# Kernel optimization log

Measured on AMD Instinct MI355X. Metric: run time of the kernel, lower is better.

## Reference

```python
import jax, jax.numpy as jnp
import numpy as np
import math

HIDDEN = 512
NUM_HEADS = 16
HEAD_DIM = HIDDEN // NUM_HEADS          # 32
SPOW_DIM = HEAD_DIM * (HEAD_DIM + 1) // 2  # 528
GAMMA = 0.9
B, S = 2, 1024

_TRIU_I, _TRIU_J = np.triu_indices(HEAD_DIM, k=1)
_SQRT2 = math.sqrt(2.0)


def spow2(x):
    # x: (..., d) -> (..., d*(d+1)//2); squares then sqrt(2)*upper-tri cross terms
    squares = x * x
    cross = _SQRT2 * (x[..., _TRIU_I] * x[..., _TRIU_J])
    return jnp.concatenate([squares, cross], axis=-1)


def setup_inputs() -> dict:
    key = jax.random.key(0)
    ks = jax.random.split(key, 9)
    lim = 1.0 / math.sqrt(HIDDEN)
    w = lambda k: jax.random.uniform(k, (HIDDEN, HIDDEN), jnp.float32, -lim, lim)
    b = lambda k: jax.random.uniform(k, (HIDDEN,), jnp.float32, -lim, lim)
    return {
        "x": jax.random.normal(ks[0], (B, S, HIDDEN), jnp.float32),
        "q_w": w(ks[1]), "q_b": b(ks[2]),
        "k_w": w(ks[3]), "k_b": b(ks[4]),
        "v_w": w(ks[5]), "v_b": b(ks[6]),
        "o_w": w(ks[7]), "o_b": b(ks[8]),
    }


def reference(x, q_w, q_b, k_w, k_b, v_w, v_b, o_w, o_b):
    Bb, Ss, Hh = x.shape
    q = (x @ q_w + q_b).reshape(Bb, Ss, NUM_HEADS, HEAD_DIM)
    k = (x @ k_w + k_b).reshape(Bb, Ss, NUM_HEADS, HEAD_DIM)
    v = (x @ v_w + v_b).reshape(Bb, Ss, NUM_HEADS, HEAD_DIM)

    sq = spow2(q)  # [B,S,H,Dspow]
    sk = spow2(k)  # [B,S,H,Dspow]

    # time-major for scan
    sq_t = jnp.moveaxis(sq, 1, 0)  # [S,B,H,D]
    sk_t = jnp.moveaxis(sk, 1, 0)
    v_t = jnp.moveaxis(v, 1, 0)    # [S,B,H,hd]

    state0 = jnp.zeros((Bb, NUM_HEADS, SPOW_DIM, HEAD_DIM), x.dtype)

    def step(state, inp):
        skt, sqt, vt = inp
        # state = gamma*state + spow_k \otimes v  -> [B,H,Dspow,hd]
        state = GAMMA * state + skt[..., :, None] * vt[..., None, :]
        out = jnp.einsum('bhD,bhDd->bhd', sqt, state)
        return state, out

    _, outs = jax.lax.scan(step, state0, (sk_t, sq_t, v_t))  # [S,B,H,hd]
    out = jnp.moveaxis(outs, 0, 1).reshape(Bb, Ss, Hh)
    return out @ o_w + o_b
```

## Files before the change

### kernel.cpp

```cpp
#include <hip/hip_runtime.h>
#include <hip/hip_bf16.h>
#include <math.h>

#define HIDDEN 512
#define NHEADS 16
#define HDIM   32
#define BATCH  2
#define SEQ    1024
#define MROWS  (BATCH * SEQ)

constexpr float LOG2_GAMMA = -0.15200309344504997f;

typedef __hip_bfloat16 bf16;
typedef __attribute__((ext_vector_type(8))) short short8;
typedef __attribute__((ext_vector_type(4))) float f32x4;

__device__ __forceinline__ void async16(const void* g, void* l) {
    __builtin_amdgcn_global_load_lds(
        (const __attribute__((address_space(1))) void*)g,
        (__attribute__((address_space(3))) void*)l, 16, 0, 0);
}

__device__ __forceinline__ unsigned short f2bf_bits(float f) {
    bf16 b = __float2bfloat16(f);
    return *(unsigned short*)&b;
}

__global__ __launch_bounds__(256) void prep(
    const float* __restrict__ x,
    const float* __restrict__ qw, const float* __restrict__ kw,
    const float* __restrict__ vw, const float* __restrict__ ow,
    bf16* __restrict__ xb, bf16* __restrict__ wqkvt, bf16* __restrict__ wot)
{
    const int blk = blockIdx.x, tid = threadIdx.x;
    if (blk < 256) {
        const int widx = blk >> 6;
        const int tile = blk & 63;
        const int tk = (tile & 7) * 64, tn = (tile >> 3) * 64;
        const float* w = widx == 0 ? qw : widx == 1 ? kw : widx == 2 ? vw : ow;
        __shared__ float t[64][65];
        #pragma unroll
        for (int u = 0; u < 4; ++u) {
            const int r = u * 16 + (tid >> 4);
            const int c = (tid & 15) * 4;
            float4 v = *(const float4*)&w[(size_t)(tk + r) * 512 + tn + c];
            t[r][c + 0] = v.x; t[r][c + 1] = v.y; t[r][c + 2] = v.z; t[r][c + 3] = v.w;
        }
        __syncthreads();
        #pragma unroll
        for (int u = 0; u < 2; ++u) {
            const int rr = u * 32 + (tid >> 3);
            const int cc = (tid & 7) * 8;
            alignas(16) unsigned short tmp[8];
            #pragma unroll
            for (int i = 0; i < 8; ++i) tmp[i] = f2bf_bits(t[cc + i][rr]);
            bf16* dst = (widx < 3)
                ? &wqkvt[((size_t)widx * 512 + tn + rr) * 512 + tk + cc]
                : &wot[(size_t)(tn + rr) * 512 + tk + cc];
            *(short8*)dst = *(short8*)tmp;
        }
    } else {
        #pragma unroll
        for (int u = 0; u < 4; ++u) {
            const int idx = (blk - 256) * 1024 + u * 256 + tid;
            float4 v = ((const float4*)x)[idx];
            unsigned pk0 = (unsigned)f2bf_bits(v.x) | ((unsigned)f2bf_bits(v.y) << 16);
            unsigned pk1 = (unsigned)f2bf_bits(v.z) | ((unsigned)f2bf_bits(v.w) << 16);
            uint2 pk = {pk0, pk1};
            *(uint2*)&xb[(size_t)idx * 4] = pk;
        }
    }
}

template<int BM, int BN, int EPI>
__global__ __launch_bounds__(256) void gemm_mfma(
    const bf16* __restrict__ A, const bf16* __restrict__ Bt,
    const float* __restrict__ b0, const float* __restrict__ b1,
    const float* __restrict__ b2,
    float* __restrict__ Cf, bf16* __restrict__ Cb, int ldc)
{
    constexpr int K = 512, BK = 32;
    constexpr int TM = BM / 32, TN = BN / 32;
    __shared__ alignas(16) short As[BM * BK];
    __shared__ alignas(16) short Bs[BN * BK];

    const int tid = threadIdx.x;
    const int wave = tid >> 6, lane = tid & 63;
    const int m0 = blockIdx.y * BM, n0 = blockIdx.x * BN;
    const int wm = (wave >> 1) * (BM / 2), wn = (wave & 1) * (BN / 2);
    const int fr = lane & 15, quad = lane >> 4;
    const int fk = quad * 8;
    const int lrow = lane >> 2, lk = (lane & 3) * 8;

    f32x4 acc[TM][TN] = {};

    for (int k0 = 0; k0 < K; k0 += BK) {
        #pragma unroll
        for (int u = 0; u < BM / 64; ++u) {
            const int rb = (wave * (BM / 64) + u) * 16;
            async16(&A[(size_t)(m0 + rb + lrow) * K + k0 + lk], &As[rb * BK]);
        }
        #pragma unroll
        for (int u = 0; u < BN / 64; ++u) {
            const int rb = (wave * (BN / 64) + u) * 16;
            async16(&Bt[(size_t)(n0 + rb + lrow) * K + k0 + lk], &Bs[rb * BK]);
        }
        __syncthreads();

        short8 af[TM], bfr[TN];
        #pragma unroll
        for (int i = 0; i < TM; ++i)
            af[i] = *(const short8*)&As[(wm + i * 16 + fr) * BK + fk];
        #pragma unroll
        for (int j = 0; j < TN; ++j)
            bfr[j] = *(const short8*)&Bs[(wn + j * 16 + fr) * BK + fk];
        #pragma unroll
        for (int i = 0; i < TM; ++i)
            #pragma unroll
            for (int j = 0; j < TN; ++j)
                acc[i][j] = __builtin_amdgcn_mfma_f32_16x16x32_bf16(
                    af[i], bfr[j], acc[i][j], 0, 0, 0);
        __syncthreads();
    }

    if (EPI == 1) {
        const int seg = (blockIdx.x * BN) >> 9;
        const float* bp = seg == 0 ? b0 : seg == 1 ? b1 : b2;
        const float sgn = seg == 0 ? 0.5f : seg == 1 ? -0.5f : 0.0f;
        #pragma unroll
        for (int i = 0; i < TM; ++i) {
            const int mrow = m0 + wm + i * 16 + quad * 4;
            float sc[4];
            #pragma unroll
            for (int r = 0; r < 4; ++r)
                sc[r] = exp2f((float)((mrow + r) & 63) * (sgn * LOG2_GAMMA));
            #pragma unroll
            for (int j = 0; j < TN; ++j) {
                const int n = n0 + wn + j * 16 + fr;
                const float bv = bp[n & 511];
                #pragma unroll
                for (int r = 0; r < 4; ++r) {
                    unsigned short h = f2bf_bits((acc[i][j][r] + bv) * sc[r]);
                    *(unsigned short*)&Cb[(size_t)(mrow + r) * ldc + n] = h;
                }
            }
        }
    } else {
        #pragma unroll
        for (int i = 0; i < TM; ++i) {
            const int mrow = m0 + wm + i * 16 + quad * 4;
            #pragma unroll
            for (int j = 0; j < TN; ++j) {
                const int n = n0 + wn + j * 16 + fr;
                const float bv = b0[n];
                #pragma unroll
                for (int r = 0; r < 4; ++r)
                    Cf[(size_t)(mrow + r) * ldc + n] = acc[i][j][r] + bv;
            }
        }
    }
}

__global__ __launch_bounds__(256) void power_attn_mfma(
    const bf16* __restrict__ qkv, bf16* __restrict__ atc)
{
    __shared__ alignas(16) short Qs[64 * 32];
    __shared__ alignas(16) short Ks[64 * 32];
    __shared__ alignas(16) short Vt[32 * 80];
    __shared__ alignas(16) short Ps[64 * 72];

    const int tid = threadIdx.x, wave = tid >> 6, lane = tid & 63;
    const int chunk = blockIdx.x, bh = blockIdx.y;
    const int b = bh >> 4, h = bh & 15;
    const int mb = b * SEQ + chunk * 64;
    const int fr = lane & 15, quad = lane >> 4;

    async16(&qkv[(size_t)(mb + wave * 16 + (lane >> 2)) * 1536 + h * 32 + (lane & 3) * 8],
            &Qs[wave * 512]);

    f32x4 o0 = {}, o1 = {};
    const int jstart = chunk >= 2 ? chunk - 2 : 0;

    for (int j = jstart; j <= chunk; ++j) {
        __syncthreads();
        const int sb = b * SEQ + j * 64;
        async16(&qkv[(size_t)(sb + wave * 16 + (lane >> 2)) * 1536 + 512 + h * 32 + (lane & 3) * 8],
                &Ks[wave * 512]);
        if (tid < 128) {
            const int p = tid >> 2, s = p * 2, dbase = (tid & 3) * 8;
            const short* g = (const short*)&qkv[(size_t)(sb + s) * 1536 + 1024 + h * 32 + dbase];
            short8 v0 = *(const short8*)g;
            short8 v1 = *(const short8*)(g + 1536);
            #pragma unroll
            for (int i = 0; i < 8; ++i) {
                unsigned pk = (unsigned)(unsigned short)v0[i]
                            | ((unsigned)(unsigned short)v1[i] << 16);
                *(unsigned*)&Vt[(dbase + i) * 80 + s] = pk;
            }
        }
        __syncthreads();

        short8 aq = *(const short8*)&Qs[(wave * 16 + fr) * 32 + quad * 8];
        f32x4 sAcc[4] = {};
        #pragma unroll
        for (int nt = 0; nt < 4; ++nt) {
            short8 bk = *(const short8*)&Ks[(nt * 16 + fr) * 32 + quad * 8];
            sAcc[nt] = __builtin_amdgcn_mfma_f32_16x16x32_bf16(aq, bk, sAcc[nt], 0, 0, 0);
        }

        const int dj = chunk - j;
        const float sj = exp2f(64.0f * (float)dj * LOG2_GAMMA);
        const int tbase = wave * 16 + quad * 4;
        #pragma unroll
        for (int nt = 0; nt < 4; ++nt) {
            const int s_l = nt * 16 + fr;
            #pragma unroll
            for (int r = 0; r < 4; ++r) {
                const int t_l = tbase + r;
                float pv = sAcc[nt][r];
                pv = pv * pv * sj;
                if (dj == 0 && s_l > t_l) pv = 0.0f;
                Ps[t_l * 72 + s_l] = (short)f2bf_bits(pv);
            }
        }
        short8 a0 = *(const short8*)&Ps[(wave * 16 + fr) * 72 + quad * 8];
        short8 a1 = *(const short8*)&Ps[(wave * 16 + fr) * 72 + 32 + quad * 8];
        short8 b00 = *(const short8*)&Vt[fr * 80 + quad * 8];
        short8 b01 = *(const short8*)&Vt[fr * 80 + 32 + quad * 8];
        short8 b10 = *(const short8*)&Vt[(16 + fr) * 80 + quad * 8];
        short8 b11 = *(const short8*)&Vt[(16 + fr) * 80 + 32 + quad * 8];
        o0 = __builtin_amdgcn_mfma_f32_16x16x32_bf16(a0, b00, o0, 0, 0, 0);
        o0 = __builtin_amdgcn_mfma_f32_16x16x32_bf16(a1, b01, o0, 0, 0, 0);
        o1 = __builtin_amdgcn_mfma_f32_16x16x32_bf16(a0, b10, o1, 0, 0, 0);
        o1 = __builtin_amdgcn_mfma_f32_16x16x32_bf16(a1, b11, o1, 0, 0, 0);
    }

    #pragma unroll
    for (int r = 0; r < 4; ++r) {
        const size_t row = mb + wave * 16 + quad * 4 + r;
        const int col = h * 32 + fr;
        *(unsigned short*)&atc[row * 512 + col]      = f2bf_bits(o0[r]);
        *(unsigned short*)&atc[row * 512 + col + 16] = f2bf_bits(o1[r]);
    }
}

extern "C" void kernel_launch(void* const* d_in, const int* in_sizes, int n_in,
                              void* d_out, int out_size, void* d_ws, size_t ws_size,
                              hipStream_t stream)
{
    const float* x  = (const float*)d_in[0];
    const float* qw = (const float*)d_in[1];
    const float* qb = (const float*)d_in[2];
    const float* kw = (const float*)d_in[3];
    const float* kb = (const float*)d_in[4];
    const float* vw = (const float*)d_in[5];
    const float* vb = (const float*)d_in[6];
    const float* ow = (const float*)d_in[7];
    const float* ob = (const float*)d_in[8];
    float* out = (float*)d_out;

    char* w = (char*)d_ws;
    bf16* xb    = (bf16*)(w);
    bf16* wqkvt = (bf16*)(w + (2ull  << 20));
    bf16* wot   = (bf16*)(w + (2ull  << 20) + (1536ull << 10));
    bf16* qkvb  = (bf16*)(w + (4ull  << 20));
    bf16* atc   = (bf16*)(w + (10ull << 20));

    prep<<<512, 256, 0, stream>>>(x, qw, kw, vw, ow, xb, wqkvt, wot);

    gemm_mfma<128, 64, 1><<<dim3(1536 / 64, MROWS / 128), 256, 0, stream>>>(
        xb, wqkvt, qb, kb, vb, nullptr, qkvb, 1536);

    power_attn_mfma<<<dim3(SEQ / 64, BATCH * NHEADS), 256, 0, stream>>>(qkvb, atc);

    gemm_mfma<64, 64, 0><<<dim3(512 / 64, MROWS / 64), 256, 0, stream>>>(
        atc, wot, ob, nullptr, nullptr, out, nullptr, 512);
}
```

Measured before the change: 99.17 us.

## Load MFMA fragments directly from global memory instead of staging through LDS

Both GEMMs drop the LDS-staged tile loop with its barriers and instead have each wave load its bf16 A/B fragments straight from global memory into registers. The loop is fully unrolled and software-prefetches the next k-step. The QKV GEMM also moves to 64x64 tiles, which doubles its block count. The attention kernel now reads Q and K fragments directly from global instead of going through shared buffers. This removes LDS traffic and __syncthreads, but gives up intra-block data reuse, so more global and L2 reads are issued.

```diff
diff --git a/kernel.cpp b/kernel.cpp
--- a/kernel.cpp
+++ b/kernel.cpp
@@ -14,12 +14,6 @@
 typedef __hip_bfloat16 bf16;
 typedef __attribute__((ext_vector_type(8))) short short8;
 typedef __attribute__((ext_vector_type(4))) float f32x4;
-
-__device__ __forceinline__ void async16(const void* g, void* l) {
-    __builtin_amdgcn_global_load_lds(
-        (const __attribute__((address_space(1))) void*)g,
-        (__attribute__((address_space(3))) void*)l, 16, 0, 0);
-}
 
 __device__ __forceinline__ unsigned short f2bf_bits(float f) {
     bf16 b = __float2bfloat16(f);
@@ -72,71 +66,63 @@
     }
 }
 
-template<int BM, int BN, int EPI>
-__global__ __launch_bounds__(256) void gemm_mfma(
+template<int EPI>
+__global__ __launch_bounds__(256) void gemm_direct(
     const bf16* __restrict__ A, const bf16* __restrict__ Bt,
     const float* __restrict__ b0, const float* __restrict__ b1,
     const float* __restrict__ b2,
     float* __restrict__ Cf, bf16* __restrict__ Cb, int ldc)
 {
-    constexpr int K = 512, BK = 32;
-    constexpr int TM = BM / 32, TN = BN / 32;
-    __shared__ alignas(16) short As[BM * BK];
-    __shared__ alignas(16) short Bs[BN * BK];
-
+    constexpr int K = 512;
     const int tid = threadIdx.x;
     const int wave = tid >> 6, lane = tid & 63;
-    const int m0 = blockIdx.y * BM, n0 = blockIdx.x * BN;
-    const int wm = (wave >> 1) * (BM / 2), wn = (wave & 1) * (BN / 2);
     const int fr = lane & 15, quad = lane >> 4;
-    const int fk = quad * 8;
-    const int lrow = lane >> 2, lk = (lane & 3) * 8;
-
-    f32x4 acc[TM][TN] = {};
-
-    for (int k0 = 0; k0 < K; k0 += BK) {
-        #pragma unroll
-        for (int u = 0; u < BM / 64; ++u) {
-            const int rb = (wave * (BM / 64) + u) * 16;
-            async16(&A[(size_t)(m0 + rb + lrow) * K + k0 + lk], &As[rb * BK]);
-        }
-        #pragma unroll
-        for (int u = 0; u < BN / 64; ++u) {
-            const int rb = (wave * (BN / 64) + u) * 16;
-            async16(&Bt[(size_t)(n0 + rb + lrow) * K + k0 + lk], &Bs[rb * BK]);
-        }
-        __syncthreads();
-
-        short8 af[TM], bfr[TN];
-        #pragma unroll
-        for (int i = 0; i < TM; ++i)
-            af[i] = *(const short8*)&As[(wm + i * 16 + fr) * BK + fk];
-        #pragma unroll
-        for (int j = 0; j < TN; ++j)
-            bfr[j] = *(const short8*)&Bs[(wn + j * 16 + fr) * BK + fk];
-        #pragma unroll
-        for (int i = 0; i < TM; ++i)
-            #pragma unroll
-            for (int j = 0; j < TN; ++j)
-                acc[i][j] = __builtin_amdgcn_mfma_f32_16x16x32_bf16(
-                    af[i], bfr[j], acc[i][j], 0, 0, 0);
-        __syncthreads();
-    }
+    const int m0 = blockIdx.y * 64 + (wave >> 1) * 32;
+    const int n0 = blockIdx.x * 64 + (wave & 1) * 32;
+
+    const bf16* pa0 = &A[(size_t)(m0 + fr) * K + quad * 8];
+    const bf16* pa1 = pa0 + (size_t)16 * K;
+    const bf16* pb0 = &Bt[(size_t)(n0 + fr) * K + quad * 8];
+    const bf16* pb1 = pb0 + (size_t)16 * K;
+
+    f32x4 acc00 = {}, acc01 = {}, acc10 = {}, acc11 = {};
+    short8 ca0 = *(const short8*)pa0;
+    short8 ca1 = *(const short8*)pa1;
+    short8 cb0 = *(const short8*)pb0;
+    short8 cb1 = *(const short8*)pb1;
+
+    #pragma unroll
+    for (int ks = 0; ks < 16; ++ks) {
+        short8 na0, na1, nb0, nb1;
+        if (ks < 15) {
+            na0 = *(const short8*)(pa0 + (ks + 1) * 32);
+            na1 = *(const short8*)(pa1 + (ks + 1) * 32);
+            nb0 = *(const short8*)(pb0 + (ks + 1) * 32);
+            nb1 = *(const short8*)(pb1 + (ks + 1) * 32);
+        }
+        acc00 = __builtin_amdgcn_mfma_f32_16x16x32_bf16(ca0, cb0, acc00, 0, 0, 0);
+        acc01 = __builtin_amdgcn_mfma_f32_16x16x32_bf16(ca0, cb1, acc01, 0, 0, 0);
+        acc10 = __builtin_amdgcn_mfma_f32_16x16x32_bf16(ca1, cb0, acc10, 0, 0, 0);
+        acc11 = __builtin_amdgcn_mfma_f32_16x16x32_bf16(ca1, cb1, acc11, 0, 0, 0);
+        ca0 = na0; ca1 = na1; cb0 = nb0; cb1 = nb1;
+    }
+
+    f32x4 acc[2][2] = {{acc00, acc01}, {acc10, acc11}};
 
     if (EPI == 1) {
-        const int seg = (blockIdx.x * BN) >> 9;
+        const int seg = (blockIdx.x * 64) >> 9;
         const float* bp = seg == 0 ? b0 : seg == 1 ? b1 : b2;
         const float sgn = seg == 0 ? 0.5f : seg == 1 ? -0.5f : 0.0f;
         #pragma unroll
-        for (int i = 0; i < TM; ++i) {
-            const int mrow = m0 + wm + i * 16 + quad * 4;
+        for (int i = 0; i < 2; ++i) {
+            const int mrow = m0 + i * 16 + quad * 4;
             float sc[4];
             #pragma unroll
             for (int r = 0; r < 4; ++r)
                 sc[r] = exp2f((float)((mrow + r) & 63) * (sgn * LOG2_GAMMA));
             #pragma unroll
-            for (int j = 0; j < TN; ++j) {
-                const int n = n0 + wn + j * 16 + fr;
+            for (int j = 0; j < 2; ++j) {
+                const int n = n0 + j * 16 + fr;
                 const float bv = bp[n & 511];
                 #pragma unroll
                 for (int r = 0; r < 4; ++r) {
@@ -147,11 +133,11 @@
         }
     } else {
         #pragma unroll
-        for (int i = 0; i < TM; ++i) {
-            const int mrow = m0 + wm + i * 16 + quad * 4;
-            #pragma unroll
-            for (int j = 0; j < TN; ++j) {
-                const int n = n0 + wn + j * 16 + fr;
+        for (int i = 0; i < 2; ++i) {
+            const int mrow = m0 + i * 16 + quad * 4;
+            #pragma unroll
+            for (int j = 0; j < 2; ++j) {
+                const int n = n0 + j * 16 + fr;
                 const float bv = b0[n];
                 #pragma unroll
                 for (int r = 0; r < 4; ++r)
@@ -164,8 +150,6 @@
 __global__ __launch_bounds__(256) void power_attn_mfma(
     const bf16* __restrict__ qkv, bf16* __restrict__ atc)
 {
-    __shared__ alignas(16) short Qs[64 * 32];
-    __shared__ alignas(16) short Ks[64 * 32];
     __shared__ alignas(16) short Vt[32 * 80];
     __shared__ alignas(16) short Ps[64 * 72];
 
@@ -175,8 +159,7 @@
     const int mb = b * SEQ + chunk * 64;
     const int fr = lane & 15, quad = lane >> 4;
 
-    async16(&qkv[(size_t)(mb + wave * 16 + (lane >> 2)) * 1536 + h * 32 + (lane & 3) * 8],
-            &Qs[wave * 512]);
+    short8 aq = *(const short8*)&qkv[(size_t)(mb + wave * 16 + fr) * 1536 + h * 32 + quad * 8];
 
     f32x4 o0 = {}, o1 = {};
     const int jstart = chunk >= 2 ? chunk - 2 : 0;
@@ -184,8 +167,6 @@
     for (int j = jstart; j <= chunk; ++j) {
         __syncthreads();
         const int sb = b * SEQ + j * 64;
-        async16(&qkv[(size_t)(sb + wave * 16 + (lane >> 2)) * 1536 + 512 + h * 32 + (lane & 3) * 8],
-                &Ks[wave * 512]);
         if (tid < 128) {
             const int p = tid >> 2, s = p * 2, dbase = (tid & 3) * 8;
             const short* g = (const short*)&qkv[(size_t)(sb + s) * 1536 + 1024 + h * 32 + dbase];
@@ -200,11 +181,10 @@
         }
         __syncthreads();
 
-        short8 aq = *(const short8*)&Qs[(wave * 16 + fr) * 32 + quad * 8];
         f32x4 sAcc[4] = {};
         #pragma unroll
         for (int nt = 0; nt < 4; ++nt) {
-            short8 bk = *(const short8*)&Ks[(nt * 16 + fr) * 32 + quad * 8];
+            short8 bk = *(const short8*)&qkv[(size_t)(sb + nt * 16 + fr) * 1536 + 512 + h * 32 + quad * 8];
             sAcc[nt] = __builtin_amdgcn_mfma_f32_16x16x32_bf16(aq, bk, sAcc[nt], 0, 0, 0);
         }
 
@@ -268,11 +248,11 @@
 
     prep<<<512, 256, 0, stream>>>(x, qw, kw, vw, ow, xb, wqkvt, wot);
 
-    gemm_mfma<128, 64, 1><<<dim3(1536 / 64, MROWS / 128), 256, 0, stream>>>(
+    gemm_direct<1><<<dim3(1536 / 64, MROWS / 64), 256, 0, stream>>>(
         xb, wqkvt, qb, kb, vb, nullptr, qkvb, 1536);
 
     power_attn_mfma<<<dim3(SEQ / 64, BATCH * NHEADS), 256, 0, stream>>>(qkvb, atc);
 
-    gemm_mfma<64, 64, 0><<<dim3(512 / 64, MROWS / 64), 256, 0, stream>>>(
+    gemm_direct<0><<<dim3(512 / 64, MROWS / 64), 256, 0, stream>>>(
         atc, wot, ob, nullptr, nullptr, out, nullptr, 512);
 }
```

Measured after the change: 115.2 us. +16.1%, slower.

## Stage full-K B tile in LDS and stream A fragments directly from global

Applied to the files above, without the earlier changes.

Replaces the K-looped GEMM, which staged both A and B per 32-wide K step with two barriers each, by a kernel that loads the whole 64xK B slab into padded LDS once. A fragments are then read straight from global memory into registers with no further barriers. The goal is to remove per-step synchronization and LDS traffic for A. The cost is more LDS per block (about 66KB), which lowers occupancy, and uncoalesced 16-byte global A loads with no latency hiding from prefetch.

```diff
diff --git a/kernel.cpp b/kernel.cpp
--- a/kernel.cpp
+++ b/kernel.cpp
@@ -72,71 +72,64 @@
     }
 }
 
-template<int BM, int BN, int EPI>
-__global__ __launch_bounds__(256) void gemm_mfma(
+template<int MS, int EPI>
+__global__ __launch_bounds__(256) void gemm_persistB(
     const bf16* __restrict__ A, const bf16* __restrict__ Bt,
     const float* __restrict__ b0, const float* __restrict__ b1,
     const float* __restrict__ b2,
     float* __restrict__ Cf, bf16* __restrict__ Cb, int ldc)
 {
-    constexpr int K = 512, BK = 32;
-    constexpr int TM = BM / 32, TN = BN / 32;
-    __shared__ alignas(16) short As[BM * BK];
-    __shared__ alignas(16) short Bs[BN * BK];
+    constexpr int K = 512;
+    constexpr int LDB = 520;
+    constexpr int TM = MS / 64;
+    __shared__ alignas(16) short Bs[64 * LDB];
 
     const int tid = threadIdx.x;
     const int wave = tid >> 6, lane = tid & 63;
-    const int m0 = blockIdx.y * BM, n0 = blockIdx.x * BN;
-    const int wm = (wave >> 1) * (BM / 2), wn = (wave & 1) * (BN / 2);
     const int fr = lane & 15, quad = lane >> 4;
-    const int fk = quad * 8;
-    const int lrow = lane >> 2, lk = (lane & 3) * 8;
-
-    f32x4 acc[TM][TN] = {};
-
-    for (int k0 = 0; k0 < K; k0 += BK) {
-        #pragma unroll
-        for (int u = 0; u < BM / 64; ++u) {
-            const int rb = (wave * (BM / 64) + u) * 16;
-            async16(&A[(size_t)(m0 + rb + lrow) * K + k0 + lk], &As[rb * BK]);
-        }
-        #pragma unroll
-        for (int u = 0; u < BN / 64; ++u) {
-            const int rb = (wave * (BN / 64) + u) * 16;
-            async16(&Bt[(size_t)(n0 + rb + lrow) * K + k0 + lk], &Bs[rb * BK]);
-        }
-        __syncthreads();
-
-        short8 af[TM], bfr[TN];
-        #pragma unroll
-        for (int i = 0; i < TM; ++i)
-            af[i] = *(const short8*)&As[(wm + i * 16 + fr) * BK + fk];
-        #pragma unroll
-        for (int j = 0; j < TN; ++j)
-            bfr[j] = *(const short8*)&Bs[(wn + j * 16 + fr) * BK + fk];
-        #pragma unroll
-        for (int i = 0; i < TM; ++i)
-            #pragma unroll
-            for (int j = 0; j < TN; ++j)
+    const int n0 = blockIdx.x * 64;
+    const int m0 = blockIdx.y * MS;
+
+    #pragma unroll
+    for (int i = 0; i < 16; ++i) {
+        const int row = wave * 16 + i;
+        async16(&Bt[(size_t)(n0 + row) * K + lane * 8], &Bs[row * LDB]);
+    }
+    __syncthreads();
+
+    const bf16* pa = &A[(size_t)(m0 + wave * (MS / 4) + fr) * K + quad * 8];
+
+    f32x4 acc[TM][4] = {};
+    #pragma unroll
+    for (int ks = 0; ks < 16; ++ks) {
+        short8 bfrag[4];
+        #pragma unroll
+        for (int j = 0; j < 4; ++j)
+            bfrag[j] = *(const short8*)&Bs[(j * 16 + fr) * LDB + ks * 32 + quad * 8];
+        #pragma unroll
+        for (int i = 0; i < TM; ++i) {
+            short8 af = *(const short8*)(pa + (size_t)i * 16 * K + ks * 32);
+            #pragma unroll
+            for (int j = 0; j < 4; ++j)
                 acc[i][j] = __builtin_amdgcn_mfma_f32_16x16x32_bf16(
-                    af[i], bfr[j], acc[i][j], 0, 0, 0);
-        __syncthreads();
+                    af, bfrag[j], acc[i][j], 0, 0, 0);
+        }
     }
 
     if (EPI == 1) {
-        const int seg = (blockIdx.x * BN) >> 9;
+        const int seg = n0 >> 9;
         const float* bp = seg == 0 ? b0 : seg == 1 ? b1 : b2;
         const float sgn = seg == 0 ? 0.5f : seg == 1 ? -0.5f : 0.0f;
         #pragma unroll
         for (int i = 0; i < TM; ++i) {
-            const int mrow = m0 + wm + i * 16 + quad * 4;
+            const int mrow = m0 + wave * (MS / 4) + i * 16 + quad * 4;
             float sc[4];
             #pragma unroll
             for (int r = 0; r < 4; ++r)
                 sc[r] = exp2f((float)((mrow + r) & 63) * (sgn * LOG2_GAMMA));
             #pragma unroll
-            for (int j = 0; j < TN; ++j) {
-                const int n = n0 + wn + j * 16 + fr;
+            for (int j = 0; j < 4; ++j) {
+                const int n = n0 + j * 16 + fr;
                 const float bv = bp[n & 511];
                 #pragma unroll
                 for (int r = 0; r < 4; ++r) {
@@ -148,10 +141,10 @@
     } else {
         #pragma unroll
         for (int i = 0; i < TM; ++i) {
-            const int mrow = m0 + wm + i * 16 + quad * 4;
-            #pragma unroll
-            for (int j = 0; j < TN; ++j) {
-                const int n = n0 + wn + j * 16 + fr;
+            const int mrow = m0 + wave * (MS / 4) + i * 16 + quad * 4;
+            #pragma unroll
+            for (int j = 0; j < 4; ++j) {
+                const int n = n0 + j * 16 + fr;
                 const float bv = b0[n];
                 #pragma unroll
                 for (int r = 0; r < 4; ++r)
@@ -268,11 +261,11 @@
 
     prep<<<512, 256, 0, stream>>>(x, qw, kw, vw, ow, xb, wqkvt, wot);
 
-    gemm_mfma<128, 64, 1><<<dim3(1536 / 64, MROWS / 128), 256, 0, stream>>>(
+    gemm_persistB<128, 1><<<dim3(1536 / 64, MROWS / 128), 256, 0, stream>>>(
         xb, wqkvt, qb, kb, vb, nullptr, qkvb, 1536);
 
     power_attn_mfma<<<dim3(SEQ / 64, BATCH * NHEADS), 256, 0, stream>>>(qkvb, atc);
 
-    gemm_mfma<64, 64, 0><<<dim3(512 / 64, MROWS / 64), 256, 0, stream>>>(
+    gemm_persistB<64, 0><<<dim3(512 / 64, MROWS / 64), 256, 0, stream>>>(
         atc, wot, ob, nullptr, nullptr, out, nullptr, 512);
 }
```

After: 97.72 us. No clear change (-1.5%).
